# Kernel optimization log

Hardware: AMD Instinct MI355X
Metric: run time of the kernel (lower is better)

The kernel has to match this reference:

```python
import jax, jax.numpy as jnp
import numpy as np

B, C, D, H, W = 2, 256, 16, 16, 16
R, G = 8, 4  # low rank r=min(8,C//4)=8, groups g=min(4,C)=4
N = D * H * W


def setup_inputs() -> dict:
    key = jax.random.key(0)
    ks = jax.random.split(key, 16)
    s = 0.05  # weight scale keeps softmax logits in a sane range
    inp = {
        'fL': jax.random.normal(ks[0], (B, C, D, H, W), jnp.float32),
        'fU': jax.random.normal(ks[1], (B, C, D, H, W), jnp.float32),
        'qL_w': jax.random.normal(ks[2], (R, C), jnp.float32) * s,
        'qL_b': jnp.zeros((R,), jnp.float32),
        'kU_w': jax.random.normal(ks[3], (R, C), jnp.float32) * s,
        'kU_b': jnp.zeros((R,), jnp.float32),
        'vU_w': jax.random.normal(ks[4], (G, C // G, C // G), jnp.float32) * s,
        'vU_b': jnp.zeros((C,), jnp.float32),
        'qU_w': jax.random.normal(ks[5], (R, C), jnp.float32) * s,
        'qU_b': jnp.zeros((R,), jnp.float32),
        'kL_w': jax.random.normal(ks[6], (R, C), jnp.float32) * s,
        'kL_b': jnp.zeros((R,), jnp.float32),
        'vL_w': jax.random.normal(ks[7], (G, C // G, C // G), jnp.float32) * s,
        'vL_b': jnp.zeros((C,), jnp.float32),
        'beta': jnp.float32(0.5),
    }
    return inp


def _conv1x1(x, w, b):
    # x: [B, C, N]; w: [O, C] (1x1x1 conv == per-voxel linear)
    return jnp.einsum('oc,bcn->bon', w, x) + b[None, :, None]


def _gconv1x1(x, w, b):
    # grouped 1x1x1 conv; x: [B, C, N]; w: [G, Cg_out, Cg_in]
    xg = x.reshape(B, G, C // G, N)
    yg = jnp.einsum('goi,bgin->bgon', w, xg)
    return yg.reshape(B, C, N) + b[None, :, None]


def _attend(q, k, v):
    # q,k: [B, R, N]; v: [B, C, N]
    attn = jax.nn.softmax(jnp.einsum('brn,brm->bnm', q, k), axis=-1)  # [B,N,N]
    return jnp.einsum('bcn,bnm->bcm', v, attn)  # bmm(v, attn)


def reference(fL, fU, qL_w, qL_b, kU_w, kU_b, vU_w, vU_b,
              qU_w, qU_b, kL_w, kL_b, vL_w, vL_b, beta):
    xL = fL.reshape(B, C, N)
    xU = fU.reshape(B, C, N)
    LU = _attend(_conv1x1(xL, qL_w, qL_b), _conv1x1(xU, kU_w, kU_b),
                 _gconv1x1(xU, vU_w, vU_b))
    UL = _attend(_conv1x1(xU, qU_w, qU_b), _conv1x1(xL, kL_w, kL_b),
                 _gconv1x1(xL, vL_w, vL_b))
    fL2 = fL + beta * LU.reshape(B, C, D, H, W)
    fU2 = fU + beta * UL.reshape(B, C, D, H, W)
    return (fL2, fU2)
```

## Files before the change

kernel.cpp:

```cpp
#include <hip/hip_runtime.h>
#include <hip/hip_bf16.h>

#define B_  2
#define C_  256
#define N_  4096
#define R_  8
#define G_  4
#define CG_ 64

typedef __attribute__((ext_vector_type(8))) short short8;
typedef __attribute__((ext_vector_type(4))) float f32x4;

#define MFMA16(a, b, c) __builtin_amdgcn_mfma_f32_16x16x32_bf16((a), (b), (c), 0, 0, 0)
#define EXP2F(x) __builtin_amdgcn_exp2f(x)
#define LOG2E 1.44269504088896f

__device__ inline unsigned int pk2(float a, float b) {
    union { __hip_bfloat162 h; unsigned int u; } cv;
    cv.h = __float22bfloat162_rn(float2{a, b});
    return cv.u;
}
__device__ inline unsigned short f2bf(float f) {
    union { __hip_bfloat16 h; unsigned short u; } cv;
    cv.h = __float2bfloat16(f);
    return cv.u;
}

#define QF_OFF   0
#define KF_OFF   524288
#define VF_OFF   1048576
#define L2Z_OFFF 2621440

#define XSTR 260
#define VTS  56

__global__ __launch_bounds__(256) void fused_pre(
    const float* __restrict__ fL, const float* __restrict__ fU,
    const float* __restrict__ qLw, const float* __restrict__ qLb,
    const float* __restrict__ kLw, const float* __restrict__ kLb,
    const float* __restrict__ vLw, const float* __restrict__ vLb,
    const float* __restrict__ qUw, const float* __restrict__ qUb,
    const float* __restrict__ kUw, const float* __restrict__ kUb,
    const float* __restrict__ vUw, const float* __restrict__ vUb,
    unsigned short* __restrict__ wsu)
{
    const int s   = blockIdx.z >> 1;
    const int b   = blockIdx.z & 1;
    const int nc0 = blockIdx.x;
    const int n0  = nc0 * 32;
    const int t   = threadIdx.x;

    const float* x  = (s ? fU : fL) + (size_t)b * C_ * N_;
    const float* wq = s ? qUw : qLw;
    const float* bq = s ? qUb : qLb;
    const float* wk = s ? kUw : kLw;
    const float* bk = s ? kUb : kLb;
    const float* wv = s ? vUw : vLw;
    const float* bv = s ? vUb : vLb;
    const int dq = s, dk = 1 - s, dv = 1 - s;

    __shared__ __align__(16) float xsf[32 * XSTR];
    __shared__ __align__(16) unsigned short vtmp[256 * VTS];
    __shared__ __align__(16) float qtmp[2][16][17];

    const int w  = t >> 6;
    const int l  = t & 63;
    const int lm = l & 15;
    const int q  = l >> 4;

    {
        const int cr   = w * 8 + (l >> 3);
        const int ncl_ = (l & 7) * 4;
        float4 xv[8];
#pragma unroll
        for (int it = 0; it < 8; it++)
            xv[it] = *reinterpret_cast<const float4*>(
                x + (size_t)(it * 32 + cr) * N_ + n0 + ncl_);
#pragma unroll
        for (int it = 0; it < 8; it++) {
            const int c = it * 32 + cr;
            xsf[(ncl_ + 0) * XSTR + c] = xv[it].x;
            xsf[(ncl_ + 1) * XSTR + c] = xv[it].y;
            xsf[(ncl_ + 2) * XSTR + c] = xv[it].z;
            xsf[(ncl_ + 3) * XSTR + c] = xv[it].w;
        }
    }
    __syncthreads();

    const int ncl = w & 1;
    const int gh  = w >> 1;
    const int nrow = ncl * 16 + lm;
    const int n = n0 + nrow;

    short8 bf[8];
    {
        const float* xr = xsf + nrow * XSTR + q * 8;
        const int kclo = (gh == 0) ? 0 : 4;
#pragma unroll
        for (int kc = 0; kc < 8; kc++) {
            if (kc < kclo) continue;
            const float4 f0 = *reinterpret_cast<const float4*>(xr + kc * 32);
            const float4 f1 = *reinterpret_cast<const float4*>(xr + kc * 32 + 4);
            union { unsigned int u[4]; short8 v; } bb;
            bb.u[0] = pk2(f0.x, f0.y); bb.u[1] = pk2(f0.z, f0.w);
            bb.u[2] = pk2(f1.x, f1.y); bb.u[3] = pk2(f1.z, f1.w);
            bf[kc] = bb.v;
        }
    }

    if (gh == 0) {
        const int o = lm;
        const float* wrow = (o < 8) ? (wq + o * C_) : (wk + (o - 8) * C_);
        const float scl = (o < 8) ? LOG2E : 1.0f;
        f32x4 pa = {0.f, 0.f, 0.f, 0.f};
#pragma unroll
        for (int kc = 0; kc < 8; kc++) {
            const float4 w0 = *reinterpret_cast<const float4*>(wrow + kc * 32 + q * 8);
            const float4 w1 = *reinterpret_cast<const float4*>(wrow + kc * 32 + q * 8 + 4);
            union { unsigned int u[4]; short8 v; } aw;
            aw.u[0] = pk2(w0.x * scl, w0.y * scl);
            aw.u[1] = pk2(w0.z * scl, w0.w * scl);
            aw.u[2] = pk2(w1.x * scl, w1.y * scl);
            aw.u[3] = pk2(w1.z * scl, w1.w * scl);
            pa = MFMA16(aw.v, bf[kc], pa);
        }
#pragma unroll
        for (int r = 0; r < 4; r++) {
            const int oo = q * 4 + r;
            qtmp[w][oo][lm] = pa[r] + ((q < 2) ? bq[oo] * LOG2E : bk[oo - 8]);
        }
        const int nt = nc0 * 2 + w;
        uint4 pq = {0u, 0u, 0u, 0u}, pk = {0u, 0u, 0u, 0u};
        if (q == 0) {
            float aq[8], ak[8];
#pragma unroll
            for (int o2 = 0; o2 < 8; o2++) { aq[o2] = qtmp[w][o2][lm]; ak[o2] = qtmp[w][8 + o2][lm]; }
            pq.x = pk2(aq[0], aq[1]); pq.y = pk2(aq[2], aq[3]);
            pq.z = pk2(aq[4], aq[5]); pq.w = pk2(aq[6], aq[7]);
            pk.x = pk2(ak[0], ak[1]); pk.y = pk2(ak[2], ak[3]);
            pk.z = pk2(ak[4], ak[5]); pk.w = pk2(ak[6], ak[7]);
        }
        *reinterpret_cast<uint4*>(wsu + QF_OFF + ((size_t)(dq * B_ + b) * 256 + nt) * 512 + l * 8) = pq;
        *reinterpret_cast<uint4*>(wsu + KF_OFF + ((size_t)(dk * B_ + b) * 256 + nt) * 512 + l * 8) = pk;
    }

    {
#pragma unroll
        for (int gi = 0; gi < 2; gi++) {
            const int g = gh * 2 + gi;
#pragma unroll
            for (int ocb = 0; ocb < 4; ocb++) {
                f32x4 ca = {0.f, 0.f, 0.f, 0.f};
#pragma unroll
                for (int kc2 = 0; kc2 < 2; kc2++) {
                    const float* wr = wv + (size_t)g * (CG_ * CG_)
                                    + (ocb * 16 + lm) * CG_ + kc2 * 32 + q * 8;
                    const float4 w0 = *reinterpret_cast<const float4*>(wr);
                    const float4 w1 = *reinterpret_cast<const float4*>(wr + 4);
                    union { unsigned int u[4]; short8 v; } aw;
                    aw.u[0] = pk2(w0.x, w0.y); aw.u[1] = pk2(w0.z, w0.w);
                    aw.u[2] = pk2(w1.x, w1.y); aw.u[3] = pk2(w1.z, w1.w);
                    ca = MFMA16(aw.v, bf[g * 2 + kc2], ca);
                }
#pragma unroll
                for (int r = 0; r < 4; r++) {
                    const int c = g * 64 + ocb * 16 + q * 4 + r;
                    vtmp[c * VTS + ncl * 16 + lm] = f2bf(ca[r] + bv[c]);
                }
            }
        }
    }
    __syncthreads();

    {
        const int db = dv * B_ + b;
#pragma unroll
        for (int ctl = 0; ctl < 4; ctl++) {
            const int ct = w * 4 + ctl;
            const uint4 v4 = *reinterpret_cast<const uint4*>(vtmp + (ct * 16 + lm) * VTS + q * 8);
            *reinterpret_cast<uint4*>(
                wsu + VF_OFF + ((size_t)(db * 16 + ct) * 128 + nc0) * 512 + l * 8) = v4;
        }
    }
}

__global__ __launch_bounds__(256) void zcalc(const unsigned short* __restrict__ wsu,
                                             float* __restrict__ wsf)
{
    const int d   = blockIdx.z;
    const int b   = blockIdx.y;
    const int nc0 = blockIdx.x;
    const int db  = d * B_ + b;
    const int t   = threadIdx.x;
    const int w   = t >> 6;
    const int l   = t & 63;
    const int lm  = l & 15;
    const int q   = l >> 4;

    const unsigned short* qF = wsu + QF_OFF + (size_t)db * 256 * 512;
    const unsigned short* kF = wsu + KF_OFF + (size_t)db * 256 * 512;

    const short8 qf0 = *reinterpret_cast<const short8*>(qF + (size_t)(nc0 * 2 + 0) * 512 + l * 8);
    const short8 qf1 = *reinterpret_cast<const short8*>(qF + (size_t)(nc0 * 2 + 1) * 512 + l * 8);

    const f32x4 zero = {0.f, 0.f, 0.f, 0.f};
    float za0[4] = {0.f, 0.f, 0.f, 0.f};
    float za1[4] = {0.f, 0.f, 0.f, 0.f};

    short8 kc_ = *reinterpret_cast<const short8*>(kF + (size_t)(w * 64) * 512 + l * 8);
    for (int it = 0; it < 64; it++) {
        const int nmt = w * 64 + ((it + 1) & 63);
        const short8 kn = *reinterpret_cast<const short8*>(kF + (size_t)nmt * 512 + l * 8);
        const f32x4 s0 = MFMA16(qf0, kc_, zero);
        const f32x4 s1 = MFMA16(qf1, kc_, zero);
#pragma unroll
        for (int r = 0; r < 4; r++) { za0[r] += EXP2F(s0[r]); za1[r] += EXP2F(s1[r]); }
        kc_ = kn;
    }

#pragma unroll
    for (int r = 0; r < 4; r++) {
        za0[r] += __shfl_xor(za0[r], 1); za0[r] += __shfl_xor(za0[r], 2);
        za0[r] += __shfl_xor(za0[r], 4); za0[r] += __shfl_xor(za0[r], 8);
        za1[r] += __shfl_xor(za1[r], 1); za1[r] += __shfl_xor(za1[r], 2);
        za1[r] += __shfl_xor(za1[r], 4); za1[r] += __shfl_xor(za1[r], 8);
    }

    __shared__ __align__(16) float zred[4][2][16];
    if (lm == 0) {
        *reinterpret_cast<float4*>(&zred[w][0][q * 4]) = float4{za0[0], za0[1], za0[2], za0[3]};
        *reinterpret_cast<float4*>(&zred[w][1][q * 4]) = float4{za1[0], za1[1], za1[2], za1[3]};
    }
    __syncthreads();
    if (t < 32) {
        const float Z = zred[0][t >> 4][t & 15] + zred[1][t >> 4][t & 15]
                      + zred[2][t >> 4][t & 15] + zred[3][t >> 4][t & 15];
        wsf[L2Z_OFFF + (size_t)db * N_ + nc0 * 32 + t] = -__log2f(Z);
    }
}

#define ESTR 136

__global__ __launch_bounds__(256) void attn_gemm(
    const float* __restrict__ fL, const float* __restrict__ fU,
    const float* __restrict__ betap,
    const unsigned short* __restrict__ wsu,
    const float* __restrict__ wsf,
    float* __restrict__ out)
{
    const int db = blockIdx.z;
    const int d  = db >> 1;
    const int b  = db & 1;
    const int t  = threadIdx.x;
    const int w  = t >> 6;
    const int l  = t & 63;
    const int lm = l & 15;
    const int q  = l >> 4;
    const int m0 = blockIdx.x * 32;

    const unsigned short* qF = wsu + QF_OFF + (size_t)db * 256 * 512;
    const unsigned short* kF = wsu + KF_OFF + (size_t)db * 256 * 512;
    const unsigned short* VF = wsu + VF_OFF + (size_t)db * 16 * 128 * 512;
    const float* l2z = wsf + L2Z_OFFF + (size_t)db * N_;
    const float* f = ((d == 0) ? fL : fU) + (size_t)b * C_ * N_;
    float*       o = out + (size_t)db * C_ * N_;

    __shared__ __align__(16) unsigned short Es[2][32 * ESTR];

    short8 kf[2];
#pragma unroll
    for (int mb = 0; mb < 2; mb++)
        kf[mb] = *reinterpret_cast<const short8*>(
            kF + (size_t)(blockIdx.x * 2 + mb) * 512 + l * 8);

    const unsigned short* Ab[4];
#pragma unroll
    for (int cb = 0; cb < 4; cb++)
        Ab[cb] = VF + (size_t)(w * 4 + cb) * 128 * 512 + l * 8;

    f32x4 acc[4][2];
#pragma unroll
    for (int cb = 0; cb < 4; cb++)
#pragma unroll
        for (int mb = 0; mb < 2; mb++) acc[cb][mb] = f32x4{0.f, 0.f, 0.f, 0.f};

    short8 A[16];
    short8 q0[2], q1[2];
    f32x4  z0[2], z1[2];

    auto loadA = [&](int i) {
        const int nc = (i & 31) * 4;
#pragma unroll
        for (int cb = 0; cb < 4; cb++)
#pragma unroll
            for (int kc = 0; kc < 4; kc++)
                A[cb * 4 + kc] = *reinterpret_cast<const short8*>(
                    Ab[cb] + (size_t)(nc + kc) * 512);
    };
    auto loadQZ = [&](short8* qA, f32x4* zf, int i) {
        const int ii = i & 31;
#pragma unroll
        for (int nc = 0; nc < 2; nc++) {
            qA[nc] = *reinterpret_cast<const short8*>(
                qF + (size_t)(ii * 8 + w * 2 + nc) * 512 + l * 8);
            zf[nc] = *reinterpret_cast<const f32x4*>(
                l2z + ii * 128 + w * 32 + nc * 16 + q * 4);
        }
    };
    auto egen = [&](const short8* qA, const f32x4* zf, unsigned short* Eb) {
#pragma unroll
        for (int mb = 0; mb < 2; mb++)
#pragma unroll
            for (int nc = 0; nc < 2; nc++) {
                const f32x4 sv = MFMA16(qA[nc], kf[mb], zf[nc]);
                uint2 p;
                p.x = pk2(EXP2F(sv[0]), EXP2F(sv[1]));
                p.y = pk2(EXP2F(sv[2]), EXP2F(sv[3]));
                *reinterpret_cast<uint2*>(
                    Eb + (mb * 16 + lm) * ESTR + w * 32 + nc * 16 + q * 4) = p;
            }
    };
    auto mainm = [&](const unsigned short* Eb) {
#pragma unroll
        for (int kc = 0; kc < 4; kc++) {
            short8 Bf[2];
#pragma unroll
            for (int mb = 0; mb < 2; mb++)
                Bf[mb] = *reinterpret_cast<const short8*>(
                    Eb + (mb * 16 + lm) * ESTR + kc * 32 + q * 8);
#pragma unroll
            for (int cb = 0; cb < 4; cb++)
#pragma unroll
                for (int mb = 0; mb < 2; mb++)
                    acc[cb][mb] = MFMA16(A[cb * 4 + kc], Bf[mb], acc[cb][mb]);
        }
    };

    loadQZ(q0, z0, 0);
    loadA(0);
    loadQZ(q1, z1, 1);

    for (int i = 0; i < 32; i += 2) {
        egen(q0, z0, Es[0]);
        __syncthreads();
        loadQZ(q0, z0, i + 2);
        mainm(Es[0]);
        loadA(i + 1);

        egen(q1, z1, Es[1]);
        __syncthreads();
        loadQZ(q1, z1, i + 3);
        mainm(Es[1]);
        loadA(i + 2);
    }

    const float beta = *betap;
#pragma unroll
    for (int cb = 0; cb < 4; cb++) {
#pragma unroll
        for (int mb = 0; mb < 2; mb++) {
            const int c = w * 64 + cb * 16 + q * 4;
            const int m = m0 + mb * 16 + lm;
#pragma unroll
            for (int r = 0; r < 4; r++) {
                const size_t off = (size_t)(c + r) * N_ + m;
                o[off] = f[off] + beta * acc[cb][mb][r];
            }
        }
    }
}

extern "C" void kernel_launch(void* const* d_in, const int* in_sizes, int n_in,
                              void* d_out, int out_size, void* d_ws, size_t ws_size,
                              hipStream_t stream)
{
    const float* fL   = (const float*)d_in[0];
    const float* fU   = (const float*)d_in[1];
    const float* qL_w = (const float*)d_in[2];
    const float* qL_b = (const float*)d_in[3];
    const float* kU_w = (const float*)d_in[4];
    const float* kU_b = (const float*)d_in[5];
    const float* vU_w = (const float*)d_in[6];
    const float* vU_b = (const float*)d_in[7];
    const float* qU_w = (const float*)d_in[8];
    const float* qU_b = (const float*)d_in[9];
    const float* kL_w = (const float*)d_in[10];
    const float* kL_b = (const float*)d_in[11];
    const float* vL_w = (const float*)d_in[12];
    const float* vL_b = (const float*)d_in[13];
    const float* beta = (const float*)d_in[14];

    unsigned short* wsu  = (unsigned short*)d_ws;
    float*          wsf  = (float*)d_ws;
    float*          outf = (float*)d_out;

    fused_pre<<<dim3(128, 1, 4), 256, 0, stream>>>(
        fL, fU, qL_w, qL_b, kL_w, kL_b, vL_w, vL_b,
        qU_w, qU_b, kU_w, kU_b, vU_w, vU_b, wsu);

    zcalc<<<dim3(128, B_, 2), 256, 0, stream>>>(wsu, wsf);

    attn_gemm<<<dim3(128, 1, 4), 256, 0, stream>>>(
        fL, fU, beta, wsu, wsf, outf);
}
```

Before: 185.5 us.

## Widen attn_gemm M tile to 64 with XCD-aware block mapping and double-buffered A

Each attn_gemm block now covers 64 output columns instead of 32, which halves the grid to 256 blocks and halves how many times the V operand is streamed from memory. Block IDs are remapped so that blocks on the same XCD share a (d,b) slice, aiming for better L2 reuse. The A and Q/Z register loads are double-buffered one iteration ahead, with a single sync per step. In exchange, register and LDS use roughly double, and with launch_bounds(256,1) occupancy falls to one block per CU, leaving less latency hiding.

Result: slower. 551.2 us (+197.1%).

```diff
diff --git a/kernel.cpp b/kernel.cpp
--- a/kernel.cpp
+++ b/kernel.cpp
@@ -90,7 +90,6 @@
     const int ncl = w & 1;
     const int gh  = w >> 1;
     const int nrow = ncl * 16 + lm;
-    const int n = n0 + nrow;
 
     short8 bf[8];
     {
@@ -241,22 +240,25 @@
 
 #define ESTR 136
 
-__global__ __launch_bounds__(256) void attn_gemm(
+__global__ __launch_bounds__(256, 1) void attn_gemm(
     const float* __restrict__ fL, const float* __restrict__ fU,
     const float* __restrict__ betap,
     const unsigned short* __restrict__ wsu,
     const float* __restrict__ wsf,
     float* __restrict__ out)
 {
-    const int db = blockIdx.z;
-    const int d  = db >> 1;
-    const int b  = db & 1;
-    const int t  = threadIdx.x;
-    const int w  = t >> 6;
-    const int l  = t & 63;
-    const int lm = l & 15;
-    const int q  = l >> 4;
-    const int m0 = blockIdx.x * 32;
+    const int id  = blockIdx.x;
+    const int xcd = id & 7;
+    const int db  = xcd >> 1;
+    const int mt  = (id >> 3) + ((xcd & 1) << 5);
+    const int d   = db >> 1;
+    const int b   = db & 1;
+    const int t   = threadIdx.x;
+    const int w   = t >> 6;
+    const int l   = t & 63;
+    const int lm  = l & 15;
+    const int q   = l >> 4;
+    const int m0  = mt * 64;
 
     const unsigned short* qF = wsu + QF_OFF + (size_t)db * 256 * 512;
     const unsigned short* kF = wsu + KF_OFF + (size_t)db * 256 * 512;
@@ -265,54 +267,53 @@
     const float* f = ((d == 0) ? fL : fU) + (size_t)b * C_ * N_;
     float*       o = out + (size_t)db * C_ * N_;
 
-    __shared__ __align__(16) unsigned short Es[2][32 * ESTR];
-
-    short8 kf[2];
-#pragma unroll
-    for (int mb = 0; mb < 2; mb++)
-        kf[mb] = *reinterpret_cast<const short8*>(
-            kF + (size_t)(blockIdx.x * 2 + mb) * 512 + l * 8);
+    __shared__ __align__(16) unsigned short Es[2][64 * ESTR];
+
+    short8 kf2[4];
+#pragma unroll
+    for (int mb = 0; mb < 4; mb++)
+        kf2[mb] = *reinterpret_cast<const short8*>(
+            kF + (size_t)(mt * 4 + mb) * 512 + l * 8);
 
     const unsigned short* Ab[4];
 #pragma unroll
     for (int cb = 0; cb < 4; cb++)
         Ab[cb] = VF + (size_t)(w * 4 + cb) * 128 * 512 + l * 8;
 
-    f32x4 acc[4][2];
+    f32x4 acc[4][4];
 #pragma unroll
     for (int cb = 0; cb < 4; cb++)
 #pragma unroll
-        for (int mb = 0; mb < 2; mb++) acc[cb][mb] = f32x4{0.f, 0.f, 0.f, 0.f};
-
-    short8 A[16];
-    short8 q0[2], q1[2];
-    f32x4  z0[2], z1[2];
-
-    auto loadA = [&](int i) {
-        const int nc = (i & 31) * 4;
+        for (int mb = 0; mb < 4; mb++) acc[cb][mb] = f32x4{0.f, 0.f, 0.f, 0.f};
+
+    short8 A[2][16];
+    short8 qv[2][2];
+    f32x4  zv[2][2];
+
+    auto loadA = [&](int buf, int i) {
+        const int nc = i * 4;
 #pragma unroll
         for (int cb = 0; cb < 4; cb++)
 #pragma unroll
             for (int kc = 0; kc < 4; kc++)
-                A[cb * 4 + kc] = *reinterpret_cast<const short8*>(
+                A[buf][cb * 4 + kc] = *reinterpret_cast<const short8*>(
                     Ab[cb] + (size_t)(nc + kc) * 512);
     };
-    auto loadQZ = [&](short8* qA, f32x4* zf, int i) {
-        const int ii = i & 31;
+    auto loadQZ = [&](int buf, int i) {
 #pragma unroll
         for (int nc = 0; nc < 2; nc++) {
-            qA[nc] = *reinterpret_cast<const short8*>(
-                qF + (size_t)(ii * 8 + w * 2 + nc) * 512 + l * 8);
-            zf[nc] = *reinterpret_cast<const f32x4*>(
-                l2z + ii * 128 + w * 32 + nc * 16 + q * 4);
+            qv[buf][nc] = *reinterpret_cast<const short8*>(
+                qF + (size_t)(i * 8 + w * 2 + nc) * 512 + l * 8);
+            zv[buf][nc] = *reinterpret_cast<const f32x4*>(
+                l2z + i * 128 + w * 32 + nc * 16 + q * 4);
         }
     };
-    auto egen = [&](const short8* qA, const f32x4* zf, unsigned short* Eb) {
-#pragma unroll
-        for (int mb = 0; mb < 2; mb++)
+    auto egen = [&](int buf, unsigned short* Eb) {
+#pragma unroll
+        for (int mb = 0; mb < 4; mb++)
 #pragma unroll
             for (int nc = 0; nc < 2; nc++) {
-                const f32x4 sv = MFMA16(qA[nc], kf[mb], zf[nc]);
+                const f32x4 sv = MFMA16(qv[buf][nc], kf2[mb], zv[buf][nc]);
                 uint2 p;
                 p.x = pk2(EXP2F(sv[0]), EXP2F(sv[1]));
                 p.y = pk2(EXP2F(sv[2]), EXP2F(sv[3]));
@@ -320,45 +321,40 @@
                     Eb + (mb * 16 + lm) * ESTR + w * 32 + nc * 16 + q * 4) = p;
             }
     };
-    auto mainm = [&](const unsigned short* Eb) {
+    auto mainm = [&](int buf, const unsigned short* Eb) {
 #pragma unroll
         for (int kc = 0; kc < 4; kc++) {
-            short8 Bf[2];
-#pragma unroll
-            for (int mb = 0; mb < 2; mb++)
+            short8 Bf[4];
+#pragma unroll
+            for (int mb = 0; mb < 4; mb++)
                 Bf[mb] = *reinterpret_cast<const short8*>(
                     Eb + (mb * 16 + lm) * ESTR + kc * 32 + q * 8);
 #pragma unroll
             for (int cb = 0; cb < 4; cb++)
 #pragma unroll
-                for (int mb = 0; mb < 2; mb++)
-                    acc[cb][mb] = MFMA16(A[cb * 4 + kc], Bf[mb], acc[cb][mb]);
+                for (int mb = 0; mb < 4; mb++)
+                    acc[cb][mb] = MFMA16(A[buf][cb * 4 + kc], Bf[mb], acc[cb][mb]);
         }
     };
 
-    loadQZ(q0, z0, 0);
-    loadA(0);
-    loadQZ(q1, z1, 1);
-
-    for (int i = 0; i < 32; i += 2) {
-        egen(q0, z0, Es[0]);
+    loadA(0, 0);
+    loadQZ(0, 0);
+
+    for (int i = 0; i < 32; i++) {
+        const int ib = i & 1;
+        unsigned short* Eb = Es[ib];
+        egen(ib, Eb);
         __syncthreads();
-        loadQZ(q0, z0, i + 2);
-        mainm(Es[0]);
-        loadA(i + 1);
-
-        egen(q1, z1, Es[1]);
-        __syncthreads();
-        loadQZ(q1, z1, i + 3);
-        mainm(Es[1]);
-        loadA(i + 2);
+        loadA(1 - ib, (i + 1) & 31);
+        loadQZ(1 - ib, (i + 1) & 31);
+        mainm(ib, Eb);
     }
 
     const float beta = *betap;
 #pragma unroll
     for (int cb = 0; cb < 4; cb++) {
 #pragma unroll
-        for (int mb = 0; mb < 2; mb++) {
+        for (int mb = 0; mb < 4; mb++) {
             const int c = w * 64 + cb * 16 + q * 4;
             const int m = m0 + mb * 16 + lm;
 #pragma unroll
@@ -400,6 +396,6 @@
 
     zcalc<<<dim3(128, B_, 2), 256, 0, stream>>>(wsu, wsf);
 
-    attn_gemm<<<dim3(128, 1, 4), 256, 0, stream>>>(
+    attn_gemm<<<dim3(256), 256, 0, stream>>>(
         fL, fU, beta, wsu, wsf, outf);
 }
```
